# Kernel tuning notes

Measured on AMD Instinct MI355X. Metric: run time of the kernel, lower is better.

The kernel has to match this reference:

```python
import jax, jax.numpy as jnp
import numpy as np

N, D, E, H, O, K = 4096, 1024, 8, 2048, 1024, 2
LOSS_COEF = 0.01


def setup_inputs() -> dict:
    key = jax.random.key(0)
    ks = jax.random.split(key, 8)
    x = jax.random.normal(ks[0], (N, D), jnp.float32)
    return {
        "x": x,
        "x_offsets": jnp.array([0, N // 2, N], jnp.int32),  # unused by forward math
        "max_seq_len": 2048,
        "group_norm": False,
        "num_groups": 8,
        "linear_dim": D // 8,
        "norm_weight": jax.random.uniform(ks[1], (D,), jnp.float32, 0.5, 1.5),
        "norm_bias": jax.random.normal(ks[2], (D,), jnp.float32) * 0.1,
        "norm_eps": 1e-5,
        "w_gate": jax.random.normal(ks[3], (D, E), jnp.float32) * (1.0 / np.sqrt(D)),
        "experts_hidden_w": jax.random.normal(ks[4], (E, H, D), jnp.float32) * 0.02,
        "experts_hidden_bias": jnp.zeros((E, H), jnp.float32),
        "experts_w": jax.random.normal(ks[5], (E, O, H), jnp.float32) * 0.02,
        "experts_bias": jnp.zeros((E, O), jnp.float32),
        "output_weight": jax.random.normal(ks[6], (D, O), jnp.float32) * 0.02,
    }


def _cv_squared(v, eps=1e-6):
    v = v.astype(jnp.float32)
    m = v.mean()
    return jnp.var(v, ddof=1) / (m * m + eps)  # torch .var() is unbiased


def reference(x, x_offsets, max_seq_len, group_norm, num_groups, linear_dim,
              norm_weight, norm_bias, norm_eps,
              w_gate, experts_hidden_w, experts_hidden_bias,
              experts_w, experts_bias, output_weight):
    # ---- input normalization (layer_norm branch; group_norm=False) ----
    if group_norm:
        xg = x.reshape(-1, num_groups, linear_dim)
        mu = xg.mean(axis=2, keepdims=True)
        var = ((xg - mu) ** 2).mean(axis=2, keepdims=True)
        xg = (xg - mu) * jax.lax.rsqrt(var + norm_eps)
        xg = xg * norm_weight[None, :, None] + norm_bias[None, :, None]
        x_norm = xg.reshape(-1, x.shape[-1])
    else:
        mu = x.mean(axis=-1, keepdims=True)
        var = ((x - mu) ** 2).mean(axis=-1, keepdims=True)  # biased, like F.layer_norm
        x_norm = (x - mu) * jax.lax.rsqrt(var + norm_eps) * norm_weight + norm_bias

    # ---- gating: clean logits (enable_noisy_gating=False), L2-normalize rows ----
    logits = x_norm @ w_gate                                  # [N, E]
    logits = logits / jnp.maximum(
        jnp.linalg.norm(logits, axis=1, keepdims=True), 1e-12)
    probs = jax.nn.softmax(logits, axis=1)                    # softmax over all experts
    _, top_idx = jax.lax.top_k(logits, K)                     # [N, K]
    gates_k = jnp.take_along_axis(probs, top_idx, axis=1)     # top-k of softmax(logits)
    rows = jnp.arange(logits.shape[0])[:, None]
    gates = jnp.zeros_like(logits).at[rows, top_idx].set(gates_k)  # [N, E] sparse gates

    # ---- load-balancing loss (train=True, non-noisy path) ----
    importance = gates.sum(axis=0)
    load = (gates > 0).sum(axis=0).astype(jnp.float32)
    loss = (_cv_squared(importance) + _cv_squared(load)) * LOSS_COEF

    # ---- expert MLPs; gates are exactly zero off top-k so masked-dense == dispatch ----
    h = jax.nn.silu(jnp.einsum('nd,ehd->enh', x_norm, experts_hidden_w)
                    + experts_hidden_bias[:, None, :])        # [E, N, H]
    eo = jnp.einsum('enh,eoh->eno', h, experts_w) + experts_bias[:, None, :]  # [E, N, O]
    y_moe = jnp.einsum('ne,eno->no', gates.astype(jnp.float32),
                       eo.astype(jnp.float32))                # fp32 combine, like index_add

    # ---- residual projection: addmm(y_moe, x, output_weight) ----
    y = y_moe + x @ output_weight
    gate_fraction = load / load.sum()
    return (y, loss, gate_fraction)
```

## Files before the change

### kernel.cpp

```cpp
#include <hip/hip_runtime.h>
#include <hip/hip_bf16.h>
#include <stdint.h>

#define N_TOK 4096
#define DIM   1024
#define NE    8
#define NH    2048
#define NO    1024

typedef __attribute__((ext_vector_type(8))) short bf16x8;
typedef __attribute__((ext_vector_type(16))) float f32x16;

__device__ inline unsigned short f2bf(float f) {
    unsigned u = __float_as_uint(f);
    u += 0x7fffu + ((u >> 16) & 1u);
    return (unsigned short)(u >> 16);
}

__device__ inline void async_copy16(const void* g, void* l) {
    __builtin_amdgcn_global_load_lds(
        (const __attribute__((address_space(1))) void*)g,
        (__attribute__((address_space(3))) void*)l, 16, 0, 0);
}

#define LN_BLK  4096
#define CVT_BLK 32768
__global__ __launch_bounds__(256) void fused_prep_kernel(
    const float* __restrict__ x, const float* __restrict__ nw,
    const float* __restrict__ nb, const float* __restrict__ eps_p,
    const float* __restrict__ wg,
    unsigned short* __restrict__ xn_bf, unsigned short* __restrict__ x_bf,
    int* __restrict__ tok_e, float* __restrict__ tok_g,
    const float* __restrict__ whw, unsigned short* __restrict__ wh_bf,
    const float* __restrict__ wow, unsigned short* __restrict__ wo_bf,
    const float* __restrict__ wout, unsigned short* __restrict__ wt_bf)
{
    __shared__ float tile[32][33];
    __shared__ float rs[4], rs2[4];
    __shared__ float gred[4][NE];

    int b = blockIdx.x, t = threadIdx.x;

    if (b < LN_BLK) {
        int n = b;
        int lane = t & 63, wv = t >> 6;

        const float4 xv = ((const float4*)(x + (size_t)n * DIM))[t];
        float s  = xv.x + xv.y + xv.z + xv.w;
        float s2 = xv.x*xv.x + xv.y*xv.y + xv.z*xv.z + xv.w*xv.w;
        #pragma unroll
        for (int o = 32; o > 0; o >>= 1) {
            s  += __shfl_down(s, o);
            s2 += __shfl_down(s2, o);
        }
        if (lane == 0) { rs[wv] = s; rs2[wv] = s2; }
        __syncthreads();
        float S  = rs[0] + rs[1] + rs[2] + rs[3];
        float S2 = rs2[0] + rs2[1] + rs2[2] + rs2[3];
        const float inv = 1.0f / (float)DIM;
        float mu = S * inv;
        float var = fmaxf(S2 * inv - mu * mu, 0.0f);
        float rstd = rsqrtf(var + eps_p[0]);

        float4 w4 = ((const float4*)nw)[t];
        float4 b4 = ((const float4*)nb)[t];
        float xn0 = (xv.x - mu) * rstd * w4.x + b4.x;
        float xn1 = (xv.y - mu) * rstd * w4.y + b4.y;
        float xn2 = (xv.z - mu) * rstd * w4.z + b4.z;
        float xn3 = (xv.w - mu) * rstd * w4.w + b4.w;

        ushort4 pn; pn.x = f2bf(xn0); pn.y = f2bf(xn1); pn.z = f2bf(xn2); pn.w = f2bf(xn3);
        ((ushort4*)(xn_bf + (size_t)n * DIM))[t] = pn;
        ushort4 px; px.x = f2bf(xv.x); px.y = f2bf(xv.y); px.z = f2bf(xv.z); px.w = f2bf(xv.w);
        ((ushort4*)(x_bf + (size_t)n * DIM))[t] = px;

        float acc[NE];
        #pragma unroll
        for (int e = 0; e < NE; ++e) acc[e] = 0.0f;
        float xns[4] = {xn0, xn1, xn2, xn3};
        const float4* wgp = (const float4*)(wg + (size_t)(4 * t) * NE);
        #pragma unroll
        for (int j = 0; j < 4; ++j) {
            float4 w0 = wgp[2 * j], w1 = wgp[2 * j + 1];
            float xj = xns[j];
            acc[0] += xj * w0.x; acc[1] += xj * w0.y; acc[2] += xj * w0.z; acc[3] += xj * w0.w;
            acc[4] += xj * w1.x; acc[5] += xj * w1.y; acc[6] += xj * w1.z; acc[7] += xj * w1.w;
        }
        #pragma unroll
        for (int o = 32; o > 0; o >>= 1) {
            #pragma unroll
            for (int e = 0; e < NE; ++e) acc[e] += __shfl_down(acc[e], o);
        }
        if (lane == 0) {
            #pragma unroll
            for (int e = 0; e < NE; ++e) gred[wv][e] = acc[e];
        }
        __syncthreads();
        if (t == 0) {
            float lg[NE];
            float nrm2 = 0.0f;
            #pragma unroll
            for (int e = 0; e < NE; ++e) {
                lg[e] = gred[0][e] + gred[1][e] + gred[2][e] + gred[3][e];
                nrm2 += lg[e] * lg[e];
            }
            float den = fmaxf(sqrtf(nrm2), 1e-12f);
            float linv = 1.0f / den;
            #pragma unroll
            for (int e = 0; e < NE; ++e) lg[e] *= linv;
            float mx = lg[0];
            #pragma unroll
            for (int e = 1; e < NE; ++e) mx = fmaxf(mx, lg[e]);
            float p[NE], ps = 0.0f;
            #pragma unroll
            for (int e = 0; e < NE; ++e) { p[e] = expf(lg[e] - mx); ps += p[e]; }
            float pinv = 1.0f / ps;
            #pragma unroll
            for (int e = 0; e < NE; ++e) p[e] *= pinv;
            int i0 = 0; float b0 = lg[0];
            #pragma unroll
            for (int e = 1; e < NE; ++e) if (lg[e] > b0) { b0 = lg[e]; i0 = e; }
            int i1 = -1; float b1 = -3.0e38f;
            #pragma unroll
            for (int e = 0; e < NE; ++e) if (e != i0 && lg[e] > b1) { b1 = lg[e]; i1 = e; }
            tok_e[2 * n] = i0; tok_e[2 * n + 1] = i1;
            tok_g[2 * n] = p[i0]; tok_g[2 * n + 1] = p[i1];
        }
        return;
    }

    int b2 = b - LN_BLK;
    if (b2 < CVT_BLK) {
        const int n4each = NE * NH * DIM / 4;
        int i = b2 * 256 + t;
        const float4* s; ushort4* d; int j;
        if (i < n4each) { s = (const float4*)whw; d = (ushort4*)wh_bf; j = i; }
        else            { s = (const float4*)wow; d = (ushort4*)wo_bf; j = i - n4each; }
        float4 v = s[j];
        ushort4 o; o.x = f2bf(v.x); o.y = f2bf(v.y); o.z = f2bf(v.z); o.w = f2bf(v.w);
        d[j] = o;
        return;
    }

    int idx = b2 - CVT_BLK;
    int o0 = (idx & 31) * 32, d0 = (idx >> 5) * 32;
    int tx = t & 31, ty0 = t >> 5;
    #pragma unroll
    for (int k = 0; k < 4; ++k) {
        int ty = ty0 + k * 8;
        tile[ty][tx] = wout[(size_t)(d0 + ty) * NO + o0 + tx];
    }
    __syncthreads();
    #pragma unroll
    for (int k = 0; k < 4; ++k) {
        int ty = ty0 + k * 8;
        wt_bf[(size_t)(o0 + ty) * DIM + d0 + tx] = f2bf(tile[tx][ty]);
    }
}

__device__ inline float cv_sq(const float* v) {
    float m = 0.0f;
    for (int e = 0; e < NE; ++e) m += v[e];
    m *= (1.0f / NE);
    float s = 0.0f;
    for (int e = 0; e < NE; ++e) { float d = v[e] - m; s += d * d; }
    s *= (1.0f / (NE - 1));
    return s / (m * m + 1e-6f);
}

__global__ __launch_bounds__(256) void routing_kernel(
    const int* __restrict__ tok_e, const float* __restrict__ tok_g,
    int* __restrict__ counts, int* __restrict__ offsets,
    int* __restrict__ rowsbuf, int* __restrict__ invslot,
    float* __restrict__ out_tail)
{
    __shared__ int   sc[4][NE], sp[4][NE];
    __shared__ float sf[4][NE];
    __shared__ int   lcur[NE];

    int rb = blockIdx.x, t = threadIdx.x;
    int lane = t & 63, wv = t >> 6;
    int chunk0 = rb * 1024;

    int lc[NE]; float li[NE];
    #pragma unroll
    for (int e = 0; e < NE; ++e) { lc[e] = 0; li[e] = 0.0f; }
    int base = t * 32;
    #pragma unroll
    for (int q = 0; q < 8; ++q) {
        int4 e4 = *(const int4*)(tok_e + base + q * 4);
        float4 g4 = *(const float4*)(tok_g + base + q * 4);
        lc[e4.x]++; li[e4.x] += g4.x;
        lc[e4.y]++; li[e4.y] += g4.y;
        lc[e4.z]++; li[e4.z] += g4.z;
        lc[e4.w]++; li[e4.w] += g4.w;
    }
    int prior_flag = (base + 32 <= chunk0) ? 1 : 0;
    int lp[NE];
    #pragma unroll
    for (int e = 0; e < NE; ++e) lp[e] = prior_flag ? lc[e] : 0;

    #pragma unroll
    for (int o = 32; o > 0; o >>= 1) {
        #pragma unroll
        for (int e = 0; e < NE; ++e) {
            lc[e] += __shfl_down(lc[e], o);
            lp[e] += __shfl_down(lp[e], o);
            li[e] += __shfl_down(li[e], o);
        }
    }
    if (lane == 0) {
        #pragma unroll
        for (int e = 0; e < NE; ++e) { sc[wv][e] = lc[e]; sp[wv][e] = lp[e]; sf[wv][e] = li[e]; }
    }
    __syncthreads();
    if (t == 0) {
        int cnt[NE], pri[NE]; float imp[NE];
        for (int e = 0; e < NE; ++e) {
            cnt[e] = sc[0][e] + sc[1][e] + sc[2][e] + sc[3][e];
            pri[e] = sp[0][e] + sp[1][e] + sp[2][e] + sp[3][e];
            imp[e] = sf[0][e] + sf[1][e] + sf[2][e] + sf[3][e];
        }
        int off = 0;
        for (int e = 0; e < NE; ++e) {
            lcur[e] = off + pri[e];
            if (rb == 0) { counts[e] = cnt[e]; offsets[e] = off; }
            off += cnt[e];
        }
        if (rb == 0) {
            float lcf[NE], lif[NE];
            for (int e = 0; e < NE; ++e) { lcf[e] = (float)cnt[e]; lif[e] = imp[e]; }
            float tot = (float)off;
            out_tail[0] = 0.01f * (cv_sq(lif) + cv_sq(lcf));
            for (int e = 0; e < NE; ++e) out_tail[1 + e] = lcf[e] / tot;
        }
    }
    __syncthreads();

    int g0 = chunk0 + 4 * t;
    int4 e4 = *(const int4*)(tok_e + g0);
    int s0 = atomicAdd(&lcur[e4.x], 1);
    int s1 = atomicAdd(&lcur[e4.y], 1);
    int s2 = atomicAdd(&lcur[e4.z], 1);
    int s3 = atomicAdd(&lcur[e4.w], 1);
    int tok0 = g0 >> 1;
    rowsbuf[s0] = tok0;     rowsbuf[s1] = tok0;
    rowsbuf[s2] = tok0 + 1; rowsbuf[s3] = tok0 + 1;
    invslot[g0]     = s0;   invslot[g0 + 1] = s1;
    invslot[g0 + 2] = s2;   invslot[g0 + 3] = s3;
}

#define BK 64

__global__ __launch_bounds__(256) void gemm1_kernel(
    const unsigned short* __restrict__ xn,
    const unsigned short* __restrict__ wh,
    const float* __restrict__ hb,
    const int* __restrict__ rowsbuf,
    const int* __restrict__ counts, const int* __restrict__ offsets,
    unsigned short* __restrict__ hbuf)
{
    int e = blockIdx.z;
    int count = counts[e];
    int tm = blockIdx.y, tn = blockIdx.x;
    if (tm * 128 >= count) return;
    int off = offsets[e];

    __shared__ alignas(16) short As[128 * BK];
    __shared__ alignas(16) short Bs[128 * BK];

    int t = threadIdx.x;
    int c = t & 7, rl = t >> 3;
    int csw = (c ^ (rl & 7)) * 8;
    const unsigned short* aptr[4];
    const unsigned short* bptr[4];
    #pragma unroll
    for (int p = 0; p < 4; ++p) {
        int mrow = tm * 128 + p * 32 + rl;
        int mc = mrow < count ? mrow : count - 1;
        int token = rowsbuf[off + mc];
        aptr[p] = xn + (size_t)token * DIM;
        bptr[p] = wh + ((size_t)e * NH + tn * 128 + p * 32 + rl) * DIM;
    }

    int lane = t & 63, wvi = t >> 6;
    int wm = (wvi & 1) * 64, wn = (wvi >> 1) * 64;
    int l31 = lane & 31, h = lane >> 5, sw = l31 & 7;

    f32x16 acc[2][2];
    #pragma unroll
    for (int i = 0; i < 2; ++i)
        #pragma unroll
        for (int j = 0; j < 2; ++j) acc[i][j] = (f32x16)(0.0f);

    for (int kt = 0; kt < DIM / BK; ++kt) {
        int kb = kt * BK + csw;
        #pragma unroll
        for (int p = 0; p < 4; ++p)
            async_copy16(aptr[p] + kb, (char*)As + p * 4096 + t * 16);
        #pragma unroll
        for (int p = 0; p < 4; ++p)
            async_copy16(bptr[p] + kb, (char*)Bs + p * 4096 + t * 16);
        __syncthreads();
        #pragma unroll
        for (int ks = 0; ks < 4; ++ks) {
            int ph = ((ks * 2 + h) ^ sw) * 8;
            bf16x8 af[2], bfr[2];
            #pragma unroll
            for (int i = 0; i < 2; ++i)
                af[i] = *(const bf16x8*)&As[(wm + i * 32 + l31) * BK + ph];
            #pragma unroll
            for (int j = 0; j < 2; ++j)
                bfr[j] = *(const bf16x8*)&Bs[(wn + j * 32 + l31) * BK + ph];
            #pragma unroll
            for (int i = 0; i < 2; ++i)
                #pragma unroll
                for (int j = 0; j < 2; ++j)
                    acc[i][j] = __builtin_amdgcn_mfma_f32_32x32x16_bf16(af[i], bfr[j], acc[i][j], 0, 0, 0);
        }
        __syncthreads();
    }

    #pragma unroll
    for (int i = 0; i < 2; ++i) {
        #pragma unroll
        for (int j = 0; j < 2; ++j) {
            int col = tn * 128 + wn + j * 32 + l31;
            float bias = hb[e * NH + col];
            #pragma unroll
            for (int r = 0; r < 16; ++r) {
                int row_d = (r & 3) + 8 * (r >> 2) + 4 * h;
                int m = tm * 128 + wm + i * 32 + row_d;
                if (m < count) {
                    float v = acc[i][j][r] + bias;
                    v = v / (1.0f + __expf(-v));
                    hbuf[(size_t)(off + m) * NH + col] = f2bf(v);
                }
            }
        }
    }
}

__global__ __launch_bounds__(256) void gemm2_kernel(
    const unsigned short* __restrict__ hbuf,
    const unsigned short* __restrict__ wo,
    const float* __restrict__ ob,
    const int* __restrict__ counts, const int* __restrict__ offsets,
    float* __restrict__ eo)
{
    int e = blockIdx.z;
    int count = counts[e];
    int tm = blockIdx.y, tn = blockIdx.x;
    if (tm * 128 >= count) return;
    int off = offsets[e];

    __shared__ alignas(16) short As[128 * BK];
    __shared__ alignas(16) short Bs[128 * BK];

    int t = threadIdx.x;
    int c = t & 7, rl = t >> 3;
    int csw = (c ^ (rl & 7)) * 8;
    const unsigned short* aptr[4];
    const unsigned short* bptr[4];
    #pragma unroll
    for (int p = 0; p < 4; ++p) {
        int mrow = tm * 128 + p * 32 + rl;
        int mc = mrow < count ? mrow : count - 1;
        aptr[p] = hbuf + (size_t)(off + mc) * NH;
        bptr[p] = wo + ((size_t)e * NO + tn * 128 + p * 32 + rl) * NH;
    }

    int lane = t & 63, wvi = t >> 6;
    int wm = (wvi & 1) * 64, wn = (wvi >> 1) * 64;
    int l31 = lane & 31, h = lane >> 5, sw = l31 & 7;

    f32x16 acc[2][2];
    #pragma unroll
    for (int i = 0; i < 2; ++i)
        #pragma unroll
        for (int j = 0; j < 2; ++j) acc[i][j] = (f32x16)(0.0f);

    for (int kt = 0; kt < NH / BK; ++kt) {
        int kb = kt * BK + csw;
        #pragma unroll
        for (int p = 0; p < 4; ++p)
            async_copy16(aptr[p] + kb, (char*)As + p * 4096 + t * 16);
        #pragma unroll
        for (int p = 0; p < 4; ++p)
            async_copy16(bptr[p] + kb, (char*)Bs + p * 4096 + t * 16);
        __syncthreads();
        #pragma unroll
        for (int ks = 0; ks < 4; ++ks) {
            int ph = ((ks * 2 + h) ^ sw) * 8;
            bf16x8 af[2], bfr[2];
            #pragma unroll
            for (int i = 0; i < 2; ++i)
                af[i] = *(const bf16x8*)&As[(wm + i * 32 + l31) * BK + ph];
            #pragma unroll
            for (int j = 0; j < 2; ++j)
                bfr[j] = *(const bf16x8*)&Bs[(wn + j * 32 + l31) * BK + ph];
            #pragma unroll
            for (int i = 0; i < 2; ++i)
                #pragma unroll
                for (int j = 0; j < 2; ++j)
                    acc[i][j] = __builtin_amdgcn_mfma_f32_32x32x16_bf16(af[i], bfr[j], acc[i][j], 0, 0, 0);
        }
        __syncthreads();
    }

    #pragma unroll
    for (int i = 0; i < 2; ++i) {
        #pragma unroll
        for (int j = 0; j < 2; ++j) {
            int col = tn * 128 + wn + j * 32 + l31;
            float bias = ob[e * NO + col];
            #pragma unroll
            for (int r = 0; r < 16; ++r) {
                int row_d = (r & 3) + 8 * (r >> 2) + 4 * h;
                int m = tm * 128 + wm + i * 32 + row_d;
                if (m < count)
                    eo[(size_t)(off + m) * NO + col] = acc[i][j][r] + bias;
            }
        }
    }
}

__global__ __launch_bounds__(256) void gemm_res_kernel(
    const unsigned short* __restrict__ xb,
    const unsigned short* __restrict__ wt,
    const float* __restrict__ eo,
    const int* __restrict__ invslot,
    const float* __restrict__ tok_g,
    float* __restrict__ y)
{
    int tm = blockIdx.y, tn = blockIdx.x;
    __shared__ alignas(16) short As[64 * BK];
    __shared__ alignas(16) short Bs[128 * BK];

    int t = threadIdx.x;
    int c = t & 7, rl = t >> 3;
    int csw = (c ^ (rl & 7)) * 8;
    const unsigned short* aptr[2];
    const unsigned short* bptr[4];
    #pragma unroll
    for (int p = 0; p < 2; ++p)
        aptr[p] = xb + (size_t)(tm * 64 + p * 32 + rl) * DIM;
    #pragma unroll
    for (int p = 0; p < 4; ++p)
        bptr[p] = wt + (size_t)(tn * 128 + p * 32 + rl) * DIM;

    int lane = t & 63, wvi = t >> 6;
    int wm = (wvi & 1) * 32, wn = (wvi >> 1) * 64;
    int l31 = lane & 31, h = lane >> 5, sw = l31 & 7;

    f32x16 acc[2];
    #pragma unroll
    for (int j = 0; j < 2; ++j) acc[j] = (f32x16)(0.0f);

    for (int kt = 0; kt < DIM / BK; ++kt) {
        int kb = kt * BK + csw;
        #pragma unroll
        for (int p = 0; p < 2; ++p)
            async_copy16(aptr[p] + kb, (char*)As + p * 4096 + t * 16);
        #pragma unroll
        for (int p = 0; p < 4; ++p)
            async_copy16(bptr[p] + kb, (char*)Bs + p * 4096 + t * 16);
        __syncthreads();
        #pragma unroll
        for (int ks = 0; ks < 4; ++ks) {
            int ph = ((ks * 2 + h) ^ sw) * 8;
            bf16x8 af, bfr[2];
            af = *(const bf16x8*)&As[(wm + l31) * BK + ph];
            #pragma unroll
            for (int j = 0; j < 2; ++j)
                bfr[j] = *(const bf16x8*)&Bs[(wn + j * 32 + l31) * BK + ph];
            #pragma unroll
            for (int j = 0; j < 2; ++j)
                acc[j] = __builtin_amdgcn_mfma_f32_32x32x16_bf16(af, bfr[j], acc[j], 0, 0, 0);
        }
        __syncthreads();
    }

    #pragma unroll
    for (int r = 0; r < 16; ++r) {
        int row_d = (r & 3) + 8 * (r >> 2) + 4 * h;
        int row = tm * 64 + wm + row_d;
        int s0 = invslot[2 * row], s1 = invslot[2 * row + 1];
        float g0 = tok_g[2 * row], g1 = tok_g[2 * row + 1];
        #pragma unroll
        for (int j = 0; j < 2; ++j) {
            int col = tn * 128 + wn + j * 32 + l31;
            y[(size_t)row * NO + col] = acc[j][r]
                + g0 * eo[(size_t)s0 * NO + col]
                + g1 * eo[(size_t)s1 * NO + col];
        }
    }
}

extern "C" void kernel_launch(void* const* d_in, const int* in_sizes, int n_in,
                              void* d_out, int out_size, void* d_ws, size_t ws_size,
                              hipStream_t stream) {
    const float* x    = (const float*)d_in[0];
    const float* nw   = (const float*)d_in[6];
    const float* nb   = (const float*)d_in[7];
    const float* eps  = (const float*)d_in[8];
    const float* wg   = (const float*)d_in[9];
    const float* whw  = (const float*)d_in[10];
    const float* whb  = (const float*)d_in[11];
    const float* wow  = (const float*)d_in[12];
    const float* wob  = (const float*)d_in[13];
    const float* wout = (const float*)d_in[14];

    char* ws = (char*)d_ws;
    unsigned short* xn_bf = (unsigned short*)(ws + 0);
    unsigned short* x_bf  = (unsigned short*)(ws + 8388608);
    unsigned short* wh_bf = (unsigned short*)(ws + 16777216);
    unsigned short* wo_bf = (unsigned short*)(ws + 50331648);
    unsigned short* wt_bf = (unsigned short*)(ws + 83886080);
    unsigned short* hbuf  = (unsigned short*)(ws + 85983232);
    float* eo = (float*)(ws + 16777216);
    char* meta = ws + 119537664;
    int*   counts     = (int*)(meta + 0);
    int*   offsets    = (int*)(meta + 128);
    int*   tok_e      = (int*)(meta + 2048);
    float* tok_g      = (float*)(meta + 2048 + 32768);
    int*   rowsbuf    = (int*)(meta + 2048 + 65536);
    int*   invslot    = (int*)(meta + 2048 + 98304);

    float* y = (float*)d_out;
    float* out_tail = y + (size_t)N_TOK * NO;

    fused_prep_kernel<<<LN_BLK + CVT_BLK + 1024, 256, 0, stream>>>(
        x, nw, nb, eps, wg, xn_bf, x_bf, tok_e, tok_g,
        whw, wh_bf, wow, wo_bf, wout, wt_bf);
    routing_kernel<<<8, 256, 0, stream>>>(
        tok_e, tok_g, counts, offsets, rowsbuf, invslot, out_tail);
    gemm1_kernel<<<dim3(NH / 128, N_TOK / 128, NE), 256, 0, stream>>>(
        xn_bf, wh_bf, whb, rowsbuf, counts, offsets, hbuf);
    gemm2_kernel<<<dim3(NO / 128, N_TOK / 128, NE), 256, 0, stream>>>(
        hbuf, wo_bf, wob, counts, offsets, eo);
    gemm_res_kernel<<<dim3(NO / 128, N_TOK / 64), 256, 0, stream>>>(
        x_bf, wt_bf, eo, invslot, tok_g, y);
}
```

Baseline: 362.6 us.

## Overlap expert-output and residual weight conversion with gemm1 via interleaved blocks

Moves the fp32-to-bf16 conversion of the second expert weights and the transpose-convert of the output weight out of the prep kernel and into the gemm1 launch. Every fifth block of the 1D grid is a GEMM tile and the others are conversion blocks. The memory-bound conversion work is meant to run alongside the compute-bound GEMM instead of before it. This costs a larger grid, div/mod index decoding, and a GEMM tile order that now walks experts by linear block id.

Result: slower. 374.1 us (+3.2%).

```diff
diff --git a/kernel.cpp b/kernel.cpp
--- a/kernel.cpp
+++ b/kernel.cpp
@@ -24,137 +24,111 @@
 }
 
 #define LN_BLK  4096
-#define CVT_BLK 32768
-__global__ __launch_bounds__(256) void fused_prep_kernel(
+#define WH_BLK  16384
+__global__ __launch_bounds__(256) void prep_a_kernel(
     const float* __restrict__ x, const float* __restrict__ nw,
     const float* __restrict__ nb, const float* __restrict__ eps_p,
     const float* __restrict__ wg,
     unsigned short* __restrict__ xn_bf, unsigned short* __restrict__ x_bf,
     int* __restrict__ tok_e, float* __restrict__ tok_g,
-    const float* __restrict__ whw, unsigned short* __restrict__ wh_bf,
-    const float* __restrict__ wow, unsigned short* __restrict__ wo_bf,
-    const float* __restrict__ wout, unsigned short* __restrict__ wt_bf)
+    const float* __restrict__ whw, unsigned short* __restrict__ wh_bf)
 {
-    __shared__ float tile[32][33];
     __shared__ float rs[4], rs2[4];
     __shared__ float gred[4][NE];
 
     int b = blockIdx.x, t = threadIdx.x;
 
-    if (b < LN_BLK) {
-        int n = b;
-        int lane = t & 63, wv = t >> 6;
-
-        const float4 xv = ((const float4*)(x + (size_t)n * DIM))[t];
-        float s  = xv.x + xv.y + xv.z + xv.w;
-        float s2 = xv.x*xv.x + xv.y*xv.y + xv.z*xv.z + xv.w*xv.w;
-        #pragma unroll
-        for (int o = 32; o > 0; o >>= 1) {
-            s  += __shfl_down(s, o);
-            s2 += __shfl_down(s2, o);
-        }
-        if (lane == 0) { rs[wv] = s; rs2[wv] = s2; }
-        __syncthreads();
-        float S  = rs[0] + rs[1] + rs[2] + rs[3];
-        float S2 = rs2[0] + rs2[1] + rs2[2] + rs2[3];
-        const float inv = 1.0f / (float)DIM;
-        float mu = S * inv;
-        float var = fmaxf(S2 * inv - mu * mu, 0.0f);
-        float rstd = rsqrtf(var + eps_p[0]);
-
-        float4 w4 = ((const float4*)nw)[t];
-        float4 b4 = ((const float4*)nb)[t];
-        float xn0 = (xv.x - mu) * rstd * w4.x + b4.x;
-        float xn1 = (xv.y - mu) * rstd * w4.y + b4.y;
-        float xn2 = (xv.z - mu) * rstd * w4.z + b4.z;
-        float xn3 = (xv.w - mu) * rstd * w4.w + b4.w;
-
-        ushort4 pn; pn.x = f2bf(xn0); pn.y = f2bf(xn1); pn.z = f2bf(xn2); pn.w = f2bf(xn3);
-        ((ushort4*)(xn_bf + (size_t)n * DIM))[t] = pn;
-        ushort4 px; px.x = f2bf(xv.x); px.y = f2bf(xv.y); px.z = f2bf(xv.z); px.w = f2bf(xv.w);
-        ((ushort4*)(x_bf + (size_t)n * DIM))[t] = px;
-
-        float acc[NE];
-        #pragma unroll
-        for (int e = 0; e < NE; ++e) acc[e] = 0.0f;
-        float xns[4] = {xn0, xn1, xn2, xn3};
-        const float4* wgp = (const float4*)(wg + (size_t)(4 * t) * NE);
-        #pragma unroll
-        for (int j = 0; j < 4; ++j) {
-            float4 w0 = wgp[2 * j], w1 = wgp[2 * j + 1];
-            float xj = xns[j];
-            acc[0] += xj * w0.x; acc[1] += xj * w0.y; acc[2] += xj * w0.z; acc[3] += xj * w0.w;
-            acc[4] += xj * w1.x; acc[5] += xj * w1.y; acc[6] += xj * w1.z; acc[7] += xj * w1.w;
-        }
-        #pragma unroll
-        for (int o = 32; o > 0; o >>= 1) {
-            #pragma unroll
-            for (int e = 0; e < NE; ++e) acc[e] += __shfl_down(acc[e], o);
-        }
-        if (lane == 0) {
-            #pragma unroll
-            for (int e = 0; e < NE; ++e) gred[wv][e] = acc[e];
-        }
-        __syncthreads();
-        if (t == 0) {
-            float lg[NE];
-            float nrm2 = 0.0f;
-            #pragma unroll
-            for (int e = 0; e < NE; ++e) {
-                lg[e] = gred[0][e] + gred[1][e] + gred[2][e] + gred[3][e];
-                nrm2 += lg[e] * lg[e];
-            }
-            float den = fmaxf(sqrtf(nrm2), 1e-12f);
-            float linv = 1.0f / den;
-            #pragma unroll
-            for (int e = 0; e < NE; ++e) lg[e] *= linv;
-            float mx = lg[0];
-            #pragma unroll
-            for (int e = 1; e < NE; ++e) mx = fmaxf(mx, lg[e]);
-            float p[NE], ps = 0.0f;
-            #pragma unroll
-            for (int e = 0; e < NE; ++e) { p[e] = expf(lg[e] - mx); ps += p[e]; }
-            float pinv = 1.0f / ps;
-            #pragma unroll
-            for (int e = 0; e < NE; ++e) p[e] *= pinv;
-            int i0 = 0; float b0 = lg[0];
-            #pragma unroll
-            for (int e = 1; e < NE; ++e) if (lg[e] > b0) { b0 = lg[e]; i0 = e; }
-            int i1 = -1; float b1 = -3.0e38f;
-            #pragma unroll
-            for (int e = 0; e < NE; ++e) if (e != i0 && lg[e] > b1) { b1 = lg[e]; i1 = e; }
-            tok_e[2 * n] = i0; tok_e[2 * n + 1] = i1;
-            tok_g[2 * n] = p[i0]; tok_g[2 * n + 1] = p[i1];
-        }
+    if (b >= LN_BLK) {
+        int i = (b - LN_BLK) * 256 + t;
+        float4 v = ((const float4*)whw)[i];
+        ushort4 o; o.x = f2bf(v.x); o.y = f2bf(v.y); o.z = f2bf(v.z); o.w = f2bf(v.w);
+        ((ushort4*)wh_bf)[i] = o;
         return;
     }
 
-    int b2 = b - LN_BLK;
-    if (b2 < CVT_BLK) {
-        const int n4each = NE * NH * DIM / 4;
-        int i = b2 * 256 + t;
-        const float4* s; ushort4* d; int j;
-        if (i < n4each) { s = (const float4*)whw; d = (ushort4*)wh_bf; j = i; }
-        else            { s = (const float4*)wow; d = (ushort4*)wo_bf; j = i - n4each; }
-        float4 v = s[j];
-        ushort4 o; o.x = f2bf(v.x); o.y = f2bf(v.y); o.z = f2bf(v.z); o.w = f2bf(v.w);
-        d[j] = o;
-        return;
-    }
-
-    int idx = b2 - CVT_BLK;
-    int o0 = (idx & 31) * 32, d0 = (idx >> 5) * 32;
-    int tx = t & 31, ty0 = t >> 5;
-    #pragma unroll
-    for (int k = 0; k < 4; ++k) {
-        int ty = ty0 + k * 8;
-        tile[ty][tx] = wout[(size_t)(d0 + ty) * NO + o0 + tx];
-    }
+    int n = b;
+    int lane = t & 63, wv = t >> 6;
+
+    const float4 xv = ((const float4*)(x + (size_t)n * DIM))[t];
+    float s  = xv.x + xv.y + xv.z + xv.w;
+    float s2 = xv.x*xv.x + xv.y*xv.y + xv.z*xv.z + xv.w*xv.w;
+    #pragma unroll
+    for (int o = 32; o > 0; o >>= 1) {
+        s  += __shfl_down(s, o);
+        s2 += __shfl_down(s2, o);
+    }
+    if (lane == 0) { rs[wv] = s; rs2[wv] = s2; }
     __syncthreads();
-    #pragma unroll
-    for (int k = 0; k < 4; ++k) {
-        int ty = ty0 + k * 8;
-        wt_bf[(size_t)(o0 + ty) * DIM + d0 + tx] = f2bf(tile[tx][ty]);
+    float S  = rs[0] + rs[1] + rs[2] + rs[3];
+    float S2 = rs2[0] + rs2[1] + rs2[2] + rs2[3];
+    const float inv = 1.0f / (float)DIM;
+    float mu = S * inv;
+    float var = fmaxf(S2 * inv - mu * mu, 0.0f);
+    float rstd = rsqrtf(var + eps_p[0]);
+
+    float4 w4 = ((const float4*)nw)[t];
+    float4 b4 = ((const float4*)nb)[t];
+    float xn0 = (xv.x - mu) * rstd * w4.x + b4.x;
+    float xn1 = (xv.y - mu) * rstd * w4.y + b4.y;
+    float xn2 = (xv.z - mu) * rstd * w4.z + b4.z;
+    float xn3 = (xv.w - mu) * rstd * w4.w + b4.w;
+
+    ushort4 pn; pn.x = f2bf(xn0); pn.y = f2bf(xn1); pn.z = f2bf(xn2); pn.w = f2bf(xn3);
+    ((ushort4*)(xn_bf + (size_t)n * DIM))[t] = pn;
+    ushort4 px; px.x = f2bf(xv.x); px.y = f2bf(xv.y); px.z = f2bf(xv.z); px.w = f2bf(xv.w);
+    ((ushort4*)(x_bf + (size_t)n * DIM))[t] = px;
+
+    float acc[NE];
+    #pragma unroll
+    for (int e = 0; e < NE; ++e) acc[e] = 0.0f;
+    float xns[4] = {xn0, xn1, xn2, xn3};
+    const float4* wgp = (const float4*)(wg + (size_t)(4 * t) * NE);
+    #pragma unroll
+    for (int j = 0; j < 4; ++j) {
+        float4 w0 = wgp[2 * j], w1 = wgp[2 * j + 1];
+        float xj = xns[j];
+        acc[0] += xj * w0.x; acc[1] += xj * w0.y; acc[2] += xj * w0.z; acc[3] += xj * w0.w;
+        acc[4] += xj * w1.x; acc[5] += xj * w1.y; acc[6] += xj * w1.z; acc[7] += xj * w1.w;
+    }
+    #pragma unroll
+    for (int o = 32; o > 0; o >>= 1) {
+        #pragma unroll
+        for (int e = 0; e < NE; ++e) acc[e] += __shfl_down(acc[e], o);
+    }
+    if (lane == 0) {
+        #pragma unroll
+        for (int e = 0; e < NE; ++e) gred[wv][e] = acc[e];
+    }
+    __syncthreads();
+    if (t == 0) {
+        float lg[NE];
+        float nrm2 = 0.0f;
+        #pragma unroll
+        for (int e = 0; e < NE; ++e) {
+            lg[e] = gred[0][e] + gred[1][e] + gred[2][e] + gred[3][e];
+            nrm2 += lg[e] * lg[e];
+        }
+        float den = fmaxf(sqrtf(nrm2), 1e-12f);
+        float linv = 1.0f / den;
+        #pragma unroll
+        for (int e = 0; e < NE; ++e) lg[e] *= linv;
+        float mx = lg[0];
+        #pragma unroll
+        for (int e = 1; e < NE; ++e) mx = fmaxf(mx, lg[e]);
+        float p[NE], ps = 0.0f;
+        #pragma unroll
+        for (int e = 0; e < NE; ++e) { p[e] = expf(lg[e] - mx); ps += p[e]; }
+        float pinv = 1.0f / ps;
+        #pragma unroll
+        for (int e = 0; e < NE; ++e) p[e] *= pinv;
+        int i0 = 0; float b0 = lg[0];
+        #pragma unroll
+        for (int e = 1; e < NE; ++e) if (lg[e] > b0) { b0 = lg[e]; i0 = e; }
+        int i1 = -1; float b1 = -3.0e38f;
+        #pragma unroll
+        for (int e = 0; e < NE; ++e) if (e != i0 && lg[e] > b1) { b1 = lg[e]; i1 = e; }
+        tok_e[2 * n] = i0; tok_e[2 * n + 1] = i1;
+        tok_g[2 * n] = p[i0]; tok_g[2 * n + 1] = p[i1];
     }
 }
 
@@ -252,24 +226,58 @@
 
 #define BK 64
 
-__global__ __launch_bounds__(256) void gemm1_kernel(
+#define G1_GRID (4096 + 16384 + 1024)
+__global__ __launch_bounds__(256) void gemm1_fused_kernel(
     const unsigned short* __restrict__ xn,
     const unsigned short* __restrict__ wh,
     const float* __restrict__ hb,
     const int* __restrict__ rowsbuf,
     const int* __restrict__ counts, const int* __restrict__ offsets,
-    unsigned short* __restrict__ hbuf)
+    unsigned short* __restrict__ hbuf,
+    const float* __restrict__ wow, unsigned short* __restrict__ wo_bf,
+    const float* __restrict__ wout, unsigned short* __restrict__ wt_bf)
 {
-    int e = blockIdx.z;
+    __shared__ alignas(16) short As[128 * BK];
+    __shared__ alignas(16) short Bs[128 * BK];
+
+    int b = blockIdx.x, t = threadIdx.x;
+    bool is_gemm = (b % 5 == 0) && (b < 4096 * 5);
+
+    if (!is_gemm) {
+        int aux = b - min((b + 4) / 5, 4096);
+        if (aux < WH_BLK) {
+            int i = aux * 256 + t;
+            float4 v = ((const float4*)wow)[i];
+            ushort4 o; o.x = f2bf(v.x); o.y = f2bf(v.y); o.z = f2bf(v.z); o.w = f2bf(v.w);
+            ((ushort4*)wo_bf)[i] = o;
+        } else {
+            float* tile = (float*)As;
+            int idx = aux - WH_BLK;
+            int o0 = (idx & 31) * 32, d0 = (idx >> 5) * 32;
+            int tx = t & 31, ty0 = t >> 5;
+            #pragma unroll
+            for (int k = 0; k < 4; ++k) {
+                int ty = ty0 + k * 8;
+                tile[ty * 33 + tx] = wout[(size_t)(d0 + ty) * NO + o0 + tx];
+            }
+            __syncthreads();
+            #pragma unroll
+            for (int k = 0; k < 4; ++k) {
+                int ty = ty0 + k * 8;
+                wt_bf[(size_t)(o0 + ty) * DIM + d0 + tx] = f2bf(tile[tx * 33 + ty]);
+            }
+        }
+        return;
+    }
+
+    int gid = b / 5;
+    int e = gid >> 9;
+    int rem = gid & 511;
+    int tm = rem >> 4, tn = rem & 15;
     int count = counts[e];
-    int tm = blockIdx.y, tn = blockIdx.x;
     if (tm * 128 >= count) return;
     int off = offsets[e];
 
-    __shared__ alignas(16) short As[128 * BK];
-    __shared__ alignas(16) short Bs[128 * BK];
-
-    int t = threadIdx.x;
     int c = t & 7, rl = t >> 3;
     int csw = (c ^ (rl & 7)) * 8;
     const unsigned short* aptr[4];
@@ -530,13 +538,13 @@
     float* y = (float*)d_out;
     float* out_tail = y + (size_t)N_TOK * NO;
 
-    fused_prep_kernel<<<LN_BLK + CVT_BLK + 1024, 256, 0, stream>>>(
-        x, nw, nb, eps, wg, xn_bf, x_bf, tok_e, tok_g,
-        whw, wh_bf, wow, wo_bf, wout, wt_bf);
+    prep_a_kernel<<<LN_BLK + WH_BLK, 256, 0, stream>>>(
+        x, nw, nb, eps, wg, xn_bf, x_bf, tok_e, tok_g, whw, wh_bf);
     routing_kernel<<<8, 256, 0, stream>>>(
         tok_e, tok_g, counts, offsets, rowsbuf, invslot, out_tail);
-    gemm1_kernel<<<dim3(NH / 128, N_TOK / 128, NE), 256, 0, stream>>>(
-        xn_bf, wh_bf, whb, rowsbuf, counts, offsets, hbuf);
+    gemm1_fused_kernel<<<G1_GRID, 256, 0, stream>>>(
+        xn_bf, wh_bf, whb, rowsbuf, counts, offsets, hbuf,
+        wow, wo_bf, wout, wt_bf);
     gemm2_kernel<<<dim3(NO / 128, N_TOK / 128, NE), 256, 0, stream>>>(
         hbuf, wo_bf, wob, counts, offsets, eo);
     gemm_res_kernel<<<dim3(NO / 128, N_TOK / 64), 256, 0, stream>>>(
```

## Convert expert weights to bf16 inside GEMM loads instead of separate pass

Applied to the files above, without the earlier changes.

Removes the standalone fp32-to-bf16 conversion pass over both expert weight tensors (128MB read, 64MB written). The GEMM kernels now load fp32 weight tiles straight into registers, pack them to bf16 and store them to LDS, in place of the async global-to-LDS copy of pre-converted bf16. The output-weight transpose moves into extra blocks of the routing kernel. The cost is that each weight tile is re-read in fp32 once per token tile (twice the bytes of bf16), and the synchronous register path loses the async copy.

New measurement: 392.5 us. 8.3% more time.

```diff
diff --git a/kernel.cpp b/kernel.cpp
--- a/kernel.cpp
+++ b/kernel.cpp
@@ -23,138 +23,108 @@
         (__attribute__((address_space(3))) void*)l, 16, 0, 0);
 }
 
-#define LN_BLK  4096
-#define CVT_BLK 32768
-__global__ __launch_bounds__(256) void fused_prep_kernel(
+__device__ inline bf16x8 pack_bf8(float4 a, float4 b) {
+    bf16x8 o;
+    o[0] = (short)f2bf(a.x); o[1] = (short)f2bf(a.y);
+    o[2] = (short)f2bf(a.z); o[3] = (short)f2bf(a.w);
+    o[4] = (short)f2bf(b.x); o[5] = (short)f2bf(b.y);
+    o[6] = (short)f2bf(b.z); o[7] = (short)f2bf(b.w);
+    return o;
+}
+
+__global__ __launch_bounds__(256) void ln_gate_kernel(
     const float* __restrict__ x, const float* __restrict__ nw,
     const float* __restrict__ nb, const float* __restrict__ eps_p,
     const float* __restrict__ wg,
     unsigned short* __restrict__ xn_bf, unsigned short* __restrict__ x_bf,
-    int* __restrict__ tok_e, float* __restrict__ tok_g,
-    const float* __restrict__ whw, unsigned short* __restrict__ wh_bf,
-    const float* __restrict__ wow, unsigned short* __restrict__ wo_bf,
-    const float* __restrict__ wout, unsigned short* __restrict__ wt_bf)
+    int* __restrict__ tok_e, float* __restrict__ tok_g)
 {
-    __shared__ float tile[32][33];
     __shared__ float rs[4], rs2[4];
     __shared__ float gred[4][NE];
 
-    int b = blockIdx.x, t = threadIdx.x;
-
-    if (b < LN_BLK) {
-        int n = b;
-        int lane = t & 63, wv = t >> 6;
-
-        const float4 xv = ((const float4*)(x + (size_t)n * DIM))[t];
-        float s  = xv.x + xv.y + xv.z + xv.w;
-        float s2 = xv.x*xv.x + xv.y*xv.y + xv.z*xv.z + xv.w*xv.w;
-        #pragma unroll
-        for (int o = 32; o > 0; o >>= 1) {
-            s  += __shfl_down(s, o);
-            s2 += __shfl_down(s2, o);
-        }
-        if (lane == 0) { rs[wv] = s; rs2[wv] = s2; }
-        __syncthreads();
-        float S  = rs[0] + rs[1] + rs[2] + rs[3];
-        float S2 = rs2[0] + rs2[1] + rs2[2] + rs2[3];
-        const float inv = 1.0f / (float)DIM;
-        float mu = S * inv;
-        float var = fmaxf(S2 * inv - mu * mu, 0.0f);
-        float rstd = rsqrtf(var + eps_p[0]);
-
-        float4 w4 = ((const float4*)nw)[t];
-        float4 b4 = ((const float4*)nb)[t];
-        float xn0 = (xv.x - mu) * rstd * w4.x + b4.x;
-        float xn1 = (xv.y - mu) * rstd * w4.y + b4.y;
-        float xn2 = (xv.z - mu) * rstd * w4.z + b4.z;
-        float xn3 = (xv.w - mu) * rstd * w4.w + b4.w;
-
-        ushort4 pn; pn.x = f2bf(xn0); pn.y = f2bf(xn1); pn.z = f2bf(xn2); pn.w = f2bf(xn3);
-        ((ushort4*)(xn_bf + (size_t)n * DIM))[t] = pn;
-        ushort4 px; px.x = f2bf(xv.x); px.y = f2bf(xv.y); px.z = f2bf(xv.z); px.w = f2bf(xv.w);
-        ((ushort4*)(x_bf + (size_t)n * DIM))[t] = px;
-
-        float acc[NE];
-        #pragma unroll
-        for (int e = 0; e < NE; ++e) acc[e] = 0.0f;
-        float xns[4] = {xn0, xn1, xn2, xn3};
-        const float4* wgp = (const float4*)(wg + (size_t)(4 * t) * NE);
-        #pragma unroll
-        for (int j = 0; j < 4; ++j) {
-            float4 w0 = wgp[2 * j], w1 = wgp[2 * j + 1];
-            float xj = xns[j];
-            acc[0] += xj * w0.x; acc[1] += xj * w0.y; acc[2] += xj * w0.z; acc[3] += xj * w0.w;
-            acc[4] += xj * w1.x; acc[5] += xj * w1.y; acc[6] += xj * w1.z; acc[7] += xj * w1.w;
-        }
-        #pragma unroll
-        for (int o = 32; o > 0; o >>= 1) {
-            #pragma unroll
-            for (int e = 0; e < NE; ++e) acc[e] += __shfl_down(acc[e], o);
-        }
-        if (lane == 0) {
-            #pragma unroll
-            for (int e = 0; e < NE; ++e) gred[wv][e] = acc[e];
-        }
-        __syncthreads();
-        if (t == 0) {
-            float lg[NE];
-            float nrm2 = 0.0f;
-            #pragma unroll
-            for (int e = 0; e < NE; ++e) {
-                lg[e] = gred[0][e] + gred[1][e] + gred[2][e] + gred[3][e];
-                nrm2 += lg[e] * lg[e];
-            }
-            float den = fmaxf(sqrtf(nrm2), 1e-12f);
-            float linv = 1.0f / den;
-            #pragma unroll
-            for (int e = 0; e < NE; ++e) lg[e] *= linv;
-            float mx = lg[0];
-            #pragma unroll
-            for (int e = 1; e < NE; ++e) mx = fmaxf(mx, lg[e]);
-            float p[NE], ps = 0.0f;
-            #pragma unroll
-            for (int e = 0; e < NE; ++e) { p[e] = expf(lg[e] - mx); ps += p[e]; }
-            float pinv = 1.0f / ps;
-            #pragma unroll
-            for (int e = 0; e < NE; ++e) p[e] *= pinv;
-            int i0 = 0; float b0 = lg[0];
-            #pragma unroll
-            for (int e = 1; e < NE; ++e) if (lg[e] > b0) { b0 = lg[e]; i0 = e; }
-            int i1 = -1; float b1 = -3.0e38f;
-            #pragma unroll
-            for (int e = 0; e < NE; ++e) if (e != i0 && lg[e] > b1) { b1 = lg[e]; i1 = e; }
-            tok_e[2 * n] = i0; tok_e[2 * n + 1] = i1;
-            tok_g[2 * n] = p[i0]; tok_g[2 * n + 1] = p[i1];
-        }
-        return;
-    }
-
-    int b2 = b - LN_BLK;
-    if (b2 < CVT_BLK) {
-        const int n4each = NE * NH * DIM / 4;
-        int i = b2 * 256 + t;
-        const float4* s; ushort4* d; int j;
-        if (i < n4each) { s = (const float4*)whw; d = (ushort4*)wh_bf; j = i; }
-        else            { s = (const float4*)wow; d = (ushort4*)wo_bf; j = i - n4each; }
-        float4 v = s[j];
-        ushort4 o; o.x = f2bf(v.x); o.y = f2bf(v.y); o.z = f2bf(v.z); o.w = f2bf(v.w);
-        d[j] = o;
-        return;
-    }
-
-    int idx = b2 - CVT_BLK;
-    int o0 = (idx & 31) * 32, d0 = (idx >> 5) * 32;
-    int tx = t & 31, ty0 = t >> 5;
-    #pragma unroll
-    for (int k = 0; k < 4; ++k) {
-        int ty = ty0 + k * 8;
-        tile[ty][tx] = wout[(size_t)(d0 + ty) * NO + o0 + tx];
-    }
+    int n = blockIdx.x, t = threadIdx.x;
+    int lane = t & 63, wv = t >> 6;
+
+    const float4 xv = ((const float4*)(x + (size_t)n * DIM))[t];
+    float s  = xv.x + xv.y + xv.z + xv.w;
+    float s2 = xv.x*xv.x + xv.y*xv.y + xv.z*xv.z + xv.w*xv.w;
+    #pragma unroll
+    for (int o = 32; o > 0; o >>= 1) {
+        s  += __shfl_down(s, o);
+        s2 += __shfl_down(s2, o);
+    }
+    if (lane == 0) { rs[wv] = s; rs2[wv] = s2; }
     __syncthreads();
-    #pragma unroll
-    for (int k = 0; k < 4; ++k) {
-        int ty = ty0 + k * 8;
-        wt_bf[(size_t)(o0 + ty) * DIM + d0 + tx] = f2bf(tile[tx][ty]);
+    float S  = rs[0] + rs[1] + rs[2] + rs[3];
+    float S2 = rs2[0] + rs2[1] + rs2[2] + rs2[3];
+    const float inv = 1.0f / (float)DIM;
+    float mu = S * inv;
+    float var = fmaxf(S2 * inv - mu * mu, 0.0f);
+    float rstd = rsqrtf(var + eps_p[0]);
+
+    float4 w4 = ((const float4*)nw)[t];
+    float4 b4 = ((const float4*)nb)[t];
+    float xn0 = (xv.x - mu) * rstd * w4.x + b4.x;
+    float xn1 = (xv.y - mu) * rstd * w4.y + b4.y;
+    float xn2 = (xv.z - mu) * rstd * w4.z + b4.z;
+    float xn3 = (xv.w - mu) * rstd * w4.w + b4.w;
+
+    ushort4 pn; pn.x = f2bf(xn0); pn.y = f2bf(xn1); pn.z = f2bf(xn2); pn.w = f2bf(xn3);
+    ((ushort4*)(xn_bf + (size_t)n * DIM))[t] = pn;
+    ushort4 px; px.x = f2bf(xv.x); px.y = f2bf(xv.y); px.z = f2bf(xv.z); px.w = f2bf(xv.w);
+    ((ushort4*)(x_bf + (size_t)n * DIM))[t] = px;
+
+    float acc[NE];
+    #pragma unroll
+    for (int e = 0; e < NE; ++e) acc[e] = 0.0f;
+    float xns[4] = {xn0, xn1, xn2, xn3};
+    const float4* wgp = (const float4*)(wg + (size_t)(4 * t) * NE);
+    #pragma unroll
+    for (int j = 0; j < 4; ++j) {
+        float4 w0 = wgp[2 * j], w1 = wgp[2 * j + 1];
+        float xj = xns[j];
+        acc[0] += xj * w0.x; acc[1] += xj * w0.y; acc[2] += xj * w0.z; acc[3] += xj * w0.w;
+        acc[4] += xj * w1.x; acc[5] += xj * w1.y; acc[6] += xj * w1.z; acc[7] += xj * w1.w;
+    }
+    #pragma unroll
+    for (int o = 32; o > 0; o >>= 1) {
+        #pragma unroll
+        for (int e = 0; e < NE; ++e) acc[e] += __shfl_down(acc[e], o);
+    }
+    if (lane == 0) {
+        #pragma unroll
+        for (int e = 0; e < NE; ++e) gred[wv][e] = acc[e];
+    }
+    __syncthreads();
+    if (t == 0) {
+        float lg[NE];
+        float nrm2 = 0.0f;
+        #pragma unroll
+        for (int e = 0; e < NE; ++e) {
+            lg[e] = gred[0][e] + gred[1][e] + gred[2][e] + gred[3][e];
+            nrm2 += lg[e] * lg[e];
+        }
+        float den = fmaxf(sqrtf(nrm2), 1e-12f);
+        float linv = 1.0f / den;
+        #pragma unroll
+        for (int e = 0; e < NE; ++e) lg[e] *= linv;
+        float mx = lg[0];
+        #pragma unroll
+        for (int e = 1; e < NE; ++e) mx = fmaxf(mx, lg[e]);
+        float p[NE], ps = 0.0f;
+        #pragma unroll
+        for (int e = 0; e < NE; ++e) { p[e] = expf(lg[e] - mx); ps += p[e]; }
+        float pinv = 1.0f / ps;
+        #pragma unroll
+        for (int e = 0; e < NE; ++e) p[e] *= pinv;
+        int i0 = 0; float b0 = lg[0];
+        #pragma unroll
+        for (int e = 1; e < NE; ++e) if (lg[e] > b0) { b0 = lg[e]; i0 = e; }
+        int i1 = -1; float b1 = -3.0e38f;
+        #pragma unroll
+        for (int e = 0; e < NE; ++e) if (e != i0 && lg[e] > b1) { b1 = lg[e]; i1 = e; }
+        tok_e[2 * n] = i0; tok_e[2 * n + 1] = i1;
+        tok_g[2 * n] = p[i0]; tok_g[2 * n + 1] = p[i1];
     }
 }
 
@@ -172,13 +142,35 @@
     const int* __restrict__ tok_e, const float* __restrict__ tok_g,
     int* __restrict__ counts, int* __restrict__ offsets,
     int* __restrict__ rowsbuf, int* __restrict__ invslot,
-    float* __restrict__ out_tail)
+    float* __restrict__ out_tail,
+    const float* __restrict__ wout, unsigned short* __restrict__ wt_bf)
 {
+    __shared__ float tile[32][33];
     __shared__ int   sc[4][NE], sp[4][NE];
     __shared__ float sf[4][NE];
     __shared__ int   lcur[NE];
 
-    int rb = blockIdx.x, t = threadIdx.x;
+    int b = blockIdx.x, t = threadIdx.x;
+
+    if (b >= 8) {
+        int idx = b - 8;
+        int o0 = (idx & 31) * 32, d0 = (idx >> 5) * 32;
+        int tx = t & 31, ty0 = t >> 5;
+        #pragma unroll
+        for (int k = 0; k < 4; ++k) {
+            int ty = ty0 + k * 8;
+            tile[ty][tx] = wout[(size_t)(d0 + ty) * NO + o0 + tx];
+        }
+        __syncthreads();
+        #pragma unroll
+        for (int k = 0; k < 4; ++k) {
+            int ty = ty0 + k * 8;
+            wt_bf[(size_t)(o0 + ty) * DIM + d0 + tx] = f2bf(tile[tx][ty]);
+        }
+        return;
+    }
+
+    int rb = b;
     int lane = t & 63, wv = t >> 6;
     int chunk0 = rb * 1024;
 
@@ -254,7 +246,7 @@
 
 __global__ __launch_bounds__(256) void gemm1_kernel(
     const unsigned short* __restrict__ xn,
-    const unsigned short* __restrict__ wh,
+    const float* __restrict__ wh,
     const float* __restrict__ hb,
     const int* __restrict__ rowsbuf,
     const int* __restrict__ counts, const int* __restrict__ offsets,
@@ -273,7 +265,7 @@
     int c = t & 7, rl = t >> 3;
     int csw = (c ^ (rl & 7)) * 8;
     const unsigned short* aptr[4];
-    const unsigned short* bptr[4];
+    const float* bptr[4];
     #pragma unroll
     for (int p = 0; p < 4; ++p) {
         int mrow = tm * 128 + p * 32 + rl;
@@ -298,9 +290,15 @@
         #pragma unroll
         for (int p = 0; p < 4; ++p)
             async_copy16(aptr[p] + kb, (char*)As + p * 4096 + t * 16);
+        float4 b0[4], b1[4];
+        #pragma unroll
+        for (int p = 0; p < 4; ++p) {
+            const float4* src = (const float4*)(bptr[p] + kb);
+            b0[p] = src[0]; b1[p] = src[1];
+        }
         #pragma unroll
         for (int p = 0; p < 4; ++p)
-            async_copy16(bptr[p] + kb, (char*)Bs + p * 4096 + t * 16);
+            *(bf16x8*)((char*)Bs + p * 4096 + t * 16) = pack_bf8(b0[p], b1[p]);
         __syncthreads();
         #pragma unroll
         for (int ks = 0; ks < 4; ++ks) {
@@ -343,7 +341,7 @@
 
 __global__ __launch_bounds__(256) void gemm2_kernel(
     const unsigned short* __restrict__ hbuf,
-    const unsigned short* __restrict__ wo,
+    const float* __restrict__ wo,
     const float* __restrict__ ob,
     const int* __restrict__ counts, const int* __restrict__ offsets,
     float* __restrict__ eo)
@@ -361,7 +359,7 @@
     int c = t & 7, rl = t >> 3;
     int csw = (c ^ (rl & 7)) * 8;
     const unsigned short* aptr[4];
-    const unsigned short* bptr[4];
+    const float* bptr[4];
     #pragma unroll
     for (int p = 0; p < 4; ++p) {
         int mrow = tm * 128 + p * 32 + rl;
@@ -385,9 +383,15 @@
         #pragma unroll
         for (int p = 0; p < 4; ++p)
             async_copy16(aptr[p] + kb, (char*)As + p * 4096 + t * 16);
+        float4 b0[4], b1[4];
+        #pragma unroll
+        for (int p = 0; p < 4; ++p) {
+            const float4* src = (const float4*)(bptr[p] + kb);
+            b0[p] = src[0]; b1[p] = src[1];
+        }
         #pragma unroll
         for (int p = 0; p < 4; ++p)
-            async_copy16(bptr[p] + kb, (char*)Bs + p * 4096 + t * 16);
+            *(bf16x8*)((char*)Bs + p * 4096 + t * 16) = pack_bf8(b0[p], b1[p]);
         __syncthreads();
         #pragma unroll
         for (int ks = 0; ks < 4; ++ks) {
@@ -514,12 +518,10 @@
     char* ws = (char*)d_ws;
     unsigned short* xn_bf = (unsigned short*)(ws + 0);
     unsigned short* x_bf  = (unsigned short*)(ws + 8388608);
-    unsigned short* wh_bf = (unsigned short*)(ws + 16777216);
-    unsigned short* wo_bf = (unsigned short*)(ws + 50331648);
-    unsigned short* wt_bf = (unsigned short*)(ws + 83886080);
-    unsigned short* hbuf  = (unsigned short*)(ws + 85983232);
-    float* eo = (float*)(ws + 16777216);
-    char* meta = ws + 119537664;
+    unsigned short* wt_bf = (unsigned short*)(ws + 16777216);
+    unsigned short* hbuf  = (unsigned short*)(ws + 18874368);
+    float*          eo    = (float*)(ws + 52428800);
+    char* meta = ws + 85983232;
     int*   counts     = (int*)(meta + 0);
     int*   offsets    = (int*)(meta + 128);
     int*   tok_e      = (int*)(meta + 2048);
@@ -530,15 +532,14 @@
     float* y = (float*)d_out;
     float* out_tail = y + (size_t)N_TOK * NO;
 
-    fused_prep_kernel<<<LN_BLK + CVT_BLK + 1024, 256, 0, stream>>>(
-        x, nw, nb, eps, wg, xn_bf, x_bf, tok_e, tok_g,
-        whw, wh_bf, wow, wo_bf, wout, wt_bf);
-    routing_kernel<<<8, 256, 0, stream>>>(
-        tok_e, tok_g, counts, offsets, rowsbuf, invslot, out_tail);
+    ln_gate_kernel<<<N_TOK, 256, 0, stream>>>(
+        x, nw, nb, eps, wg, xn_bf, x_bf, tok_e, tok_g);
+    routing_kernel<<<8 + 1024, 256, 0, stream>>>(
+        tok_e, tok_g, counts, offsets, rowsbuf, invslot, out_tail, wout, wt_bf);
     gemm1_kernel<<<dim3(NH / 128, N_TOK / 128, NE), 256, 0, stream>>>(
-        xn_bf, wh_bf, whb, rowsbuf, counts, offsets, hbuf);
+        xn_bf, whw, whb, rowsbuf, counts, offsets, hbuf);
     gemm2_kernel<<<dim3(NO / 128, N_TOK / 128, NE), 256, 0, stream>>>(
-        hbuf, wo_bf, wob, counts, offsets, eo);
+        hbuf, wow, wob, counts, offsets, eo);
     gemm_res_kernel<<<dim3(NO / 128, N_TOK / 64), 256, 0, stream>>>(
         x_bf, wt_bf, eo, invslot, tok_g, y);
 }
```
